# Kernel tuning notes

Hardware: AMD Instinct MI355X
Metric: run time of the kernel (lower is better)

Reference implementation:

```python
import jax, jax.numpy as jnp
import numpy as np


def _bin_ids(start, length, S, P):
    # For adaptive max pool, output bin i over a region of length L covers
    # [floor(i*L/P), ceil((i+1)*L/P)). Adjacent bins overlap by at most one
    # element (when L >= P), so element h belongs to bins A(h)..B(h) with
    #   A(h) = floor(h*P/L),  B(h) = ceil((h+1)*P/L) - 1,  B - A <= 1.
    # Out-of-region positions are dumped into segment P.
    pos = jnp.arange(S, dtype=start.dtype)               # (S,)
    local = pos[None, :] - start[:, None]                # (N, S) local coord
    L = length[:, None]                                  # (N, 1)
    valid = (local >= 0) & (local < L)
    idA = jnp.where(valid, (local * P) // L, P)
    idB = jnp.where(valid, -((-((local + 1) * P)) // L) - 1, P)
    return idA, idB


def _roi_pool(feature_map, rois, PH, PW):
    C, H, W = feature_map.shape
    y, x, rH, rW = rois[:, 0], rois[:, 1], rois[:, 2], rois[:, 3]

    # ---- pool rows: (C,H,W) -> (N, PH, C, W) ----
    idA_h, idB_h = _bin_ids(y, rH, H, PH)                # (N, H) each
    fm_hcw = jnp.transpose(feature_map, (1, 0, 2))       # (H, C, W)
    seg_h = lambda ids: jax.ops.segment_max(fm_hcw, ids, num_segments=PH + 1)
    pooled_h = jnp.maximum(jax.vmap(seg_h)(idA_h), jax.vmap(seg_h)(idB_h))[:, :PH]

    # ---- pool cols: (N, PH, C, W) -> (N, PW, PH, C) ----
    idA_w, idB_w = _bin_ids(x, rW, W, PW)                # (N, W) each
    data_w = jnp.transpose(pooled_h, (0, 3, 1, 2))       # (N, W, PH, C)
    seg_w = lambda d, ids: jax.ops.segment_max(d, ids, num_segments=PW + 1)
    pooled = jnp.maximum(jax.vmap(seg_w)(data_w, idA_w),
                         jax.vmap(seg_w)(data_w, idB_w))[:, :PW]
    return jnp.transpose(pooled, (0, 3, 2, 1))           # (N, C, PH, PW)


def setup_inputs() -> dict:
    key = jax.random.key(0)
    k1, k2, k3, k4, k5 = jax.random.split(key, 5)
    C, H, W, N, PH, PW = 256, 128, 128, 256, 8, 8
    feature_map = jax.random.normal(k1, (C, H, W), dtype=jnp.float32)
    # valid ROIs: rH >= PH, rW >= PW, fully in-bounds
    rH = jax.random.randint(k2, (N,), PH, H + 1, dtype=jnp.int32)
    rW = jax.random.randint(k3, (N,), PW, W + 1, dtype=jnp.int32)
    y = (jax.random.uniform(k4, (N,)) * (H - rH + 1).astype(jnp.float32)).astype(jnp.int32)
    x = (jax.random.uniform(k5, (N,)) * (W - rW + 1).astype(jnp.float32)).astype(jnp.int32)
    rois = jnp.stack([y, x, rH, rW], axis=1)
    return {"feature_map": feature_map, "rois": rois, "PH": PH, "PW": PW}


def reference(feature_map, rois, PH, PW):
    return _roi_pool(feature_map, rois, PH, PW)
```

## Files before the change

kernel.cpp:

```cpp
#include <hip/hip_runtime.h>
#include <math.h>

#define C_ 256
#define H_ 128
#define W_ 128
#define PH_ 8
#define PW_ 8
#define HW_ (H_ * W_)
#define M3ROWS (H_ - 8 + 1)

typedef unsigned short u16;
typedef u16 u16x4 __attribute__((ext_vector_type(4)));
typedef u16 u16x8 __attribute__((ext_vector_type(8)));

__device__ __forceinline__ u16x8 kmax(u16x8 a, u16x8 b) {
    return __builtin_elementwise_max(a, b);
}

__device__ __forceinline__ u16 f32_to_key(float f) {
    unsigned u = __float_as_uint(f);
    unsigned r = (u + 0x7fffu + ((u >> 16) & 1u)) >> 16;
    u16 b = (u16)r;
    return (b & 0x8000u) ? (u16)~b : (u16)(b | 0x8000u);
}
__device__ __forceinline__ float key_to_f32(u16 k) {
    u16 b = (k & 0x8000u) ? (u16)(k & 0x7fffu) : (u16)~k;
    return __uint_as_float(((unsigned)b) << 16);
}

__global__ __launch_bounds__(256) void transpose_kernel(
    const float* __restrict__ fm, u16* __restrict__ fmt)
{
    __shared__ float tile[32 * 257];
    const int tid = threadIdx.x;
    const int g   = blockIdx.x & 7;
    const int hwb = blockIdx.x >> 3;
    const int c0  = g * 32;
    const int hw0 = hwb * 256;

    const int l    = tid & 63;
    const int crow = tid >> 6;
    const int sw   = (l >> 3) & 3;
    #pragma unroll
    for (int k = 0; k < 8; ++k) {
        const int c = crow + 4 * k;
        const float4 v = *(const float4*)(fm + (size_t)(c0 + c) * HW_ + hw0 + 4 * l);
        float* t = tile + c * 257 + 4 * l;
        t[(0 + sw) & 3] = v.x;
        t[(1 + sw) & 3] = v.y;
        t[(2 + sw) & 3] = v.z;
        t[(3 + sw) & 3] = v.w;
    }
    __syncthreads();

    u16* dst = fmt + (size_t)g * HW_ * 32;
    const int cq  = tid & 7;
    const int hwr = tid >> 3;
    #pragma unroll
    for (int m = 0; m < 8; ++m) {
        const int hw = hwr + 32 * m;
        const int o  = (hw & ~3) | (((hw & 3) + m) & 3);
        u16x4 w;
        w.x = f32_to_key(tile[(4 * cq + 0) * 257 + o]);
        w.y = f32_to_key(tile[(4 * cq + 1) * 257 + o]);
        w.z = f32_to_key(tile[(4 * cq + 2) * 257 + o]);
        w.w = f32_to_key(tile[(4 * cq + 3) * 257 + o]);
        *(u16x4*)(dst + (size_t)(hw0 + hw) * 32 + 4 * cq) = w;
    }
}

__device__ __forceinline__ void vslide_body(
    const u16* __restrict__ src, u16* __restrict__ dst, int bid)
{
    const int g    = bid & 7;
    const int band = (bid >> 3) & 7;
    const int seg  = bid >> 6;
    const int i0   = band * 16;
    const int t    = threadIdx.x;
    const int co   = (t & 3) << 3;
    const int w    = (t >> 2) + 64 * seg;

    const u16* s = src + (size_t)g * HW_ * 32;
    u16*       d = dst + (size_t)g * HW_ * 32;
    const size_t RS = (size_t)W_ * 32;
    const size_t cofs = (size_t)w * 32 + co;

    u16x8 r[8];
    #pragma unroll
    for (int k = 0; k < 7; ++k)
        r[k] = *(const u16x8*)(s + (size_t)(i0 + k) * RS + cofs);
    #pragma unroll
    for (int j = 0; j < 16; ++j) {
        const int i = i0 + j;
        if (i < M3ROWS) {
            r[(j + 7) & 7] = *(const u16x8*)(s + (size_t)(i + 7) * RS + cofs);
            u16x8 m01 = kmax(r[0], r[1]);
            u16x8 m23 = kmax(r[2], r[3]);
            u16x8 m45 = kmax(r[4], r[5]);
            u16x8 m67 = kmax(r[6], r[7]);
            *(u16x8*)(d + (size_t)i * RS + cofs) =
                kmax(kmax(m01, m23), kmax(m45, m67));
        }
    }
}

__device__ __forceinline__ void mw_body(
    const u16* __restrict__ src, u16* __restrict__ dst, int mbid)
{
    const int g     = mbid & 7;
    const int hband = (mbid >> 3) & 1;
    const int jseg  = mbid >> 4;
    const int t     = threadIdx.x;
    const int co    = (t & 3) << 3;
    const int h     = hband * 64 + (t >> 2);

    const int j0   = jseg * 31;
    const int jcnt = min(31, M3ROWS - j0);

    const size_t RS = (size_t)W_ * 32;
    const u16* s = src + (size_t)g * HW_ * 32 + (size_t)h * RS + co;
    u16*       d = dst + (size_t)g * HW_ * 32 + (size_t)h * RS + co;

    u16x8 r[8];
    #pragma unroll
    for (int k = 0; k < 7; ++k)
        r[k] = *(const u16x8*)(s + (size_t)(j0 + k) * 32);
    #pragma unroll
    for (int jj = 0; jj < 31; ++jj) {
        if (jj < jcnt) {
            r[(jj + 7) & 7] = *(const u16x8*)(s + (size_t)(j0 + jj + 7) * 32);
            u16x8 m01 = kmax(r[0], r[1]);
            u16x8 m23 = kmax(r[2], r[3]);
            u16x8 m45 = kmax(r[4], r[5]);
            u16x8 m67 = kmax(r[6], r[7]);
            *(u16x8*)(d + (size_t)(j0 + jj) * 32) =
                kmax(kmax(m01, m23), kmax(m45, m67));
        }
    }
}

__global__ __launch_bounds__(256) void k2_kernel(
    const u16* __restrict__ fmt, u16* __restrict__ m3, u16* __restrict__ mw)
{
    const int bid = blockIdx.x;
    if (bid < 128) vslide_body(fmt, m3, bid);
    else           mw_body(fmt, mw, bid - 128);
}

__global__ __launch_bounds__(256) void k3_kernel(
    const u16* __restrict__ mw, u16* __restrict__ m8)
{
    vslide_body(mw, m8, blockIdx.x);
}

__global__ __launch_bounds__(256) void pool2_kernel(
    const u16* __restrict__ tabs, const int* __restrict__ rois,
    float* __restrict__ out, int N)
{
    const int bid  = blockIdx.x;
    const int cg   = bid & 7;
    const int n    = bid >> 3;
    const int w    = threadIdx.x >> 6;
    const int lane = threadIdx.x & 63;
    const int ph   = lane >> 3;
    const int pw   = lane & 7;
    const int co   = w << 3;

    const int4 roi = ((const int4*)rois)[n];
    const int y = roi.x, x = roi.y, rH = roi.z, rW = roi.w;

    const int hs  = (ph * rH) >> 3;
    const int he  = ((ph + 1) * rH + 7) >> 3;
    const int ws_ = (pw * rW) >> 3;
    const int we  = ((pw + 1) * rW + 7) >> 3;
    const int a = y + hs, b = y + he, L = he - hs;
    const int wa = x + ws_, wb = x + we, Wd = we - ws_;

    const size_t T  = (size_t)HW_ * C_;
    const size_t RS = (size_t)W_ * 32;
    const u16* pl = tabs + (size_t)cg * (HW_ * 32) + co;

    const int rsp = (L >= 8), csp = (Wd >= 8);
    const int rn = rsp ? ((L > 16) ? 3 : 2) : L;
    const int cn = csp ? ((Wd > 16) ? 3 : 2) : Wd;
    const u16* tab = pl + (size_t)rsp * T + (size_t)(csp * 2) * T;

    u16x8 acc = {0, 0, 0, 0, 0, 0, 0, 0};
    for (int r = 0; r < rn; ++r) {
        const int row = rsp ? ((r == 0) ? a : (r == 1) ? (b - 8) : (a + 5))
                            : (a + r);
        const u16* rp = tab + (size_t)row * RS;
        for (int c = 0; c < cn; ++c) {
            const int col = csp ? ((c == 0) ? wa : (c == 1) ? (wb - 8) : (wa + 5))
                                : (wa + c);
            acc = kmax(acc, *(const u16x8*)(rp + (size_t)col * 32));
        }
    }

    __shared__ float lds[2048];
    float* lp = lds + (w << 9);
    #pragma unroll
    for (int i = 0; i < 8; ++i) lp[i * 64 + lane] = key_to_f32(acc[i]);
    __syncthreads();
    const float4* lp4 = (const float4*)lds + (w << 7);
    float4* ob4 = (float4*)(out + ((size_t)n * C_ + (cg << 5) + co) * (PH_ * PW_));
    ob4[lane]      = lp4[lane];
    ob4[64 + lane] = lp4[64 + lane];
}

__global__ __launch_bounds__(256) void roi_pool_fallback(
    const float* __restrict__ fm, const int* __restrict__ rois,
    float* __restrict__ out, int N)
{
    const int wid  = threadIdx.x >> 6;
    const int lane = threadIdx.x & 63;
    const int bid  = blockIdx.x;
    const int xcd  = bid & 7;
    const int t    = bid >> 3;
    const int csub = t & 7;
    const int n    = t >> 3;
    if (n >= N) return;
    const int c = (xcd << 5) + (csub << 2) + wid;

    const int4 roi = ((const int4*)rois)[n];
    const int y = roi.x, x = roi.y, rH = roi.z, rW = roi.w;

    const float2* plane2 = (const float2*)(fm + (size_t)c * (H_ * W_));
    const int pw = lane & 7;
    const int j  = lane >> 3;
    const int ws = (pw * rW) >> 3;
    const int we = (((pw + 1) * rW) + 7) >> 3;

    #pragma unroll
    for (int ph = 0; ph < PH_; ++ph) {
        const int hs = (ph * rH) >> 3;
        const int he = ((ph + 1) * rH + 7) >> 3;
        const float2* p = plane2 + (size_t)(y + hs) * (W_ / 2) + lane;
        float m0 = -INFINITY, m1 = -INFINITY;
        int cnt = he - hs;
        while (cnt >= 2) {
            const float2 a = p[0];
            const float2 b = p[W_ / 2];
            p += W_; cnt -= 2;
            m0 = fmaxf(m0, fmaxf(a.x, b.x));
            m1 = fmaxf(m1, fmaxf(a.y, b.y));
        }
        if (cnt) { const float2 a = p[0]; m0 = fmaxf(m0, a.x); m1 = fmaxf(m1, a.y); }

        float rr = -INFINITY;
        #pragma unroll
        for (int k = 0; k < 3; ++k) {
            const int w  = ws + j + k * 8;
            const int wa = x + w;
            const float a = __shfl(m0, (wa >> 1) & 63, 64);
            const float b = __shfl(m1, (wa >> 1) & 63, 64);
            if (w < we) rr = fmaxf(rr, (wa & 1) ? b : a);
        }
        rr = fmaxf(rr, __shfl_xor(rr, 8, 64));
        rr = fmaxf(rr, __shfl_xor(rr, 16, 64));
        rr = fmaxf(rr, __shfl_xor(rr, 32, 64));
        if (lane < PW_) out[(((size_t)n * C_ + c) * PH_ + ph) * PW_ + lane] = rr;
    }
}

extern "C" void kernel_launch(void* const* d_in, const int* in_sizes, int n_in,
                              void* d_out, int out_size, void* d_ws, size_t ws_size,
                              hipStream_t stream) {
    const float* fm   = (const float*)d_in[0];
    const int*   rois = (const int*)d_in[1];
    float*       out  = (float*)d_out;
    const int N = in_sizes[1] / 4;

    const size_t Tel  = (size_t)HW_ * C_;
    const size_t need = 4 * Tel * sizeof(u16);
    if (ws_size >= need) {
        u16* fmt = (u16*)d_ws;
        u16* m3  = fmt + Tel;
        u16* mw  = fmt + 2 * Tel;
        u16* m8  = fmt + 3 * Tel;
        transpose_kernel<<<dim3((HW_ / 256) * 8), 256, 0, stream>>>(fm, fmt);
        k2_kernel<<<dim3(192), 256, 0, stream>>>(fmt, m3, mw);
        k3_kernel<<<dim3(128), 256, 0, stream>>>(mw, m8);
        pool2_kernel<<<dim3(N * 8), 256, 0, stream>>>(fmt, rois, out, N);
    } else {
        roi_pool_fallback<<<dim3(64 * N), 256, 0, stream>>>(fm, rois, out, N);
    }
}
```

Before: 111.9 us.

## Fuse horizontal 8-wide max into transpose kernel and merge slide kernels

The transpose kernel now keeps each block's two converted rows in shared memory and computes the horizontal 8-wide sliding max (mw) directly, so the separate mw pass no longer re-reads fmt from global memory. Because mw is produced earlier, the vertical slides producing m3 and m8 run in a single launch, removing one kernel launch and one dependency barrier. The cost is extra shared memory (16 KB of keys) and some integer division in the transpose kernel, which may reduce its occupancy.

```diff
diff --git a/kernel.cpp b/kernel.cpp
--- a/kernel.cpp
+++ b/kernel.cpp
@@ -28,10 +28,11 @@
     return __uint_as_float(((unsigned)b) << 16);
 }
 
-__global__ __launch_bounds__(256) void transpose_kernel(
-    const float* __restrict__ fm, u16* __restrict__ fmt)
+__global__ __launch_bounds__(256) void transpose_mw_kernel(
+    const float* __restrict__ fm, u16* __restrict__ fmt, u16* __restrict__ mw)
 {
     __shared__ float tile[32 * 257];
+    __shared__ u16 keys[256 * 32];
     const int tid = threadIdx.x;
     const int g   = blockIdx.x & 7;
     const int hwb = blockIdx.x >> 3;
@@ -66,6 +67,23 @@
         w.z = f32_to_key(tile[(4 * cq + 2) * 257 + o]);
         w.w = f32_to_key(tile[(4 * cq + 3) * 257 + o]);
         *(u16x4*)(dst + (size_t)(hw0 + hw) * 32 + 4 * cq) = w;
+        *(u16x4*)(keys + hw * 32 + 4 * cq) = w;
+    }
+    __syncthreads();
+
+    u16* mwp = mw + (size_t)g * HW_ * 32;
+    const int row0 = hwb * 2;
+    for (int o = tid; o < 968; o += 256) {
+        const int oct  = o & 3;
+        const int cell = o >> 2;
+        const int row  = cell / 121;
+        const int j    = cell - row * 121;
+        const u16* kp = keys + (row * W_ + j) * 32 + oct * 8;
+        u16x8 m = *(const u16x8*)kp;
+        #pragma unroll
+        for (int d = 1; d < 8; ++d)
+            m = kmax(m, *(const u16x8*)(kp + d * 32));
+        *(u16x8*)(mwp + (size_t)((row0 + row) * W_ + j) * 32 + oct * 8) = m;
     }
 }
 
@@ -104,53 +122,13 @@
     }
 }
 
-__device__ __forceinline__ void mw_body(
-    const u16* __restrict__ src, u16* __restrict__ dst, int mbid)
-{
-    const int g     = mbid & 7;
-    const int hband = (mbid >> 3) & 1;
-    const int jseg  = mbid >> 4;
-    const int t     = threadIdx.x;
-    const int co    = (t & 3) << 3;
-    const int h     = hband * 64 + (t >> 2);
-
-    const int j0   = jseg * 31;
-    const int jcnt = min(31, M3ROWS - j0);
-
-    const size_t RS = (size_t)W_ * 32;
-    const u16* s = src + (size_t)g * HW_ * 32 + (size_t)h * RS + co;
-    u16*       d = dst + (size_t)g * HW_ * 32 + (size_t)h * RS + co;
-
-    u16x8 r[8];
-    #pragma unroll
-    for (int k = 0; k < 7; ++k)
-        r[k] = *(const u16x8*)(s + (size_t)(j0 + k) * 32);
-    #pragma unroll
-    for (int jj = 0; jj < 31; ++jj) {
-        if (jj < jcnt) {
-            r[(jj + 7) & 7] = *(const u16x8*)(s + (size_t)(j0 + jj + 7) * 32);
-            u16x8 m01 = kmax(r[0], r[1]);
-            u16x8 m23 = kmax(r[2], r[3]);
-            u16x8 m45 = kmax(r[4], r[5]);
-            u16x8 m67 = kmax(r[6], r[7]);
-            *(u16x8*)(d + (size_t)(j0 + jj) * 32) =
-                kmax(kmax(m01, m23), kmax(m45, m67));
-        }
-    }
-}
-
-__global__ __launch_bounds__(256) void k2_kernel(
-    const u16* __restrict__ fmt, u16* __restrict__ m3, u16* __restrict__ mw)
+__global__ __launch_bounds__(256) void slides_kernel(
+    const u16* __restrict__ fmt, const u16* __restrict__ mw,
+    u16* __restrict__ m3, u16* __restrict__ m8)
 {
     const int bid = blockIdx.x;
     if (bid < 128) vslide_body(fmt, m3, bid);
-    else           mw_body(fmt, mw, bid - 128);
-}
-
-__global__ __launch_bounds__(256) void k3_kernel(
-    const u16* __restrict__ mw, u16* __restrict__ m8)
-{
-    vslide_body(mw, m8, blockIdx.x);
+    else           vslide_body(mw, m8, bid - 128);
 }
 
 __global__ __launch_bounds__(256) void pool2_kernel(
@@ -278,9 +256,8 @@
         u16* m3  = fmt + Tel;
         u16* mw  = fmt + 2 * Tel;
         u16* m8  = fmt + 3 * Tel;
-        transpose_kernel<<<dim3((HW_ / 256) * 8), 256, 0, stream>>>(fm, fmt);
-        k2_kernel<<<dim3(192), 256, 0, stream>>>(fmt, m3, mw);
-        k3_kernel<<<dim3(128), 256, 0, stream>>>(mw, m8);
+        transpose_mw_kernel<<<dim3((HW_ / 256) * 8), 256, 0, stream>>>(fm, fmt, mw);
+        slides_kernel<<<dim3(256), 256, 0, stream>>>(fmt, mw, m3, m8);
         pool2_kernel<<<dim3(N * 8), 256, 0, stream>>>(fmt, rois, out, N);
     } else {
         roi_pool_fallback<<<dim3(64 * N), 256, 0, stream>>>(fm, rois, out, N);
```

Result: faster. 104.3 us (-6.8%).
